# Optimization experiments

Hardware: AMD Instinct MI355X
Metric: run time of the kernel (lower is better)

The kernel has to match this reference:

```python
import jax, jax.numpy as jnp
import numpy as np

# DeformConv hyperparameters (from init_kwargs)
KH, KW = 3, 3
STRIDE, PAD, DIL = 1, 1, 1
GROUPS, DG = 1, 1  # groups=1, deformable_groups=1
B, C, H, W = 4, 64, 128, 128
O = 64
HO = (H + 2 * PAD - (DIL * (KH - 1) + 1)) // STRIDE + 1  # 128
WO = (W + 2 * PAD - (DIL * (KW - 1) + 1)) // STRIDE + 1  # 128


def setup_inputs() -> dict:
    key = jax.random.key(0)
    k1, k2, k3, k4 = jax.random.split(key, 4)
    x = jax.random.normal(k1, (B, C, H, W), dtype=jnp.float32)
    # offset channels: dg * K * 2, ordered (y, x) per kernel tap (DCNv1 CUDA layout)
    offset = jax.random.normal(k2, (B, 2 * DG * KH * KW, HO, WO), dtype=jnp.float32)
    fan_in = C * KH * KW
    weight = jax.random.normal(k3, (O, C // GROUPS, KH, KW), dtype=jnp.float32) / np.sqrt(fan_in)
    bias = jax.random.normal(k4, (O,), dtype=jnp.float32) * 0.01
    return {"x": x, "offset": offset, "weight": weight, "bias": bias}


def _deform_sample(x, offset):
    """Bilinear-sample x at deformed kernel tap locations.
    Returns [B, C, K, HO, WO] where K = KH*KW."""
    K = KH * KW
    Cg = C // DG
    # offset -> [B, DG, K, 2, HO, WO]; channel layout: dg*2*K, pairs (y, x)
    off = offset.reshape(B, DG, K, 2, HO, WO)
    off_y, off_x = off[:, :, :, 0], off[:, :, :, 1]  # [B, DG, K, HO, WO]

    ki = (jnp.arange(K) // KW).astype(jnp.float32)  # kernel row
    kj = (jnp.arange(K) % KW).astype(jnp.float32)   # kernel col
    base_h = (jnp.arange(HO) * STRIDE - PAD).astype(jnp.float32)
    base_w = (jnp.arange(WO) * STRIDE - PAD).astype(jnp.float32)

    # sampling positions [B, DG, K, HO, WO]
    py = off_y + (ki * DIL)[None, None, :, None, None] + base_h[None, None, None, :, None]
    px = off_x + (kj * DIL)[None, None, :, None, None] + base_w[None, None, None, None, :]

    y0f = jnp.floor(py)
    x0f = jnp.floor(px)
    ly = py - y0f
    lx = px - x0f
    hy = 1.0 - ly
    hx = 1.0 - lx
    y0 = y0f.astype(jnp.int32)
    x0 = x0f.astype(jnp.int32)
    y1 = y0 + 1
    x1 = x0 + 1

    flat = x.reshape(B, DG, Cg, H * W)

    def gather(yi, xi, wgt):
        valid = (yi >= 0) & (yi < H) & (xi >= 0) & (xi < W)
        idx = jnp.clip(yi, 0, H - 1) * W + jnp.clip(xi, 0, W - 1)
        idx = idx.reshape(B, DG, 1, K * HO * WO)
        v = jnp.take_along_axis(flat, idx, axis=-1).reshape(B, DG, Cg, K, HO, WO)
        return v * (wgt * valid.astype(wgt.dtype))[:, :, None]

    val = (gather(y0, x0, hy * hx) + gather(y0, x1, hy * lx)
           + gather(y1, x0, ly * hx) + gather(y1, x1, ly * lx))
    return val.reshape(B, C, K, HO, WO)


def reference(x, offset, weight, bias):
    sampled = _deform_sample(x, offset)              # [B, C, K, HO, WO]
    w = weight.reshape(O, C, KH * KW)                # groups = 1
    out = jnp.einsum('bckhw,ock->bohw', sampled, w)  # im2col + GEMM
    return out + bias[None, :, None, None]
```

## Files before the change

### kernel.cpp

```cpp
#include <hip/hip_runtime.h>
#include <hip/hip_fp16.h>


#define B_  4
#define C_  64
#define H_  128
#define W_  128
#define O_  64
#define HO_ 128
#define WO_ 128
#define NCHUNK 8
#define NGW 12
#define KSTEPS 3
#define NT_ 32
#define NROW 2
#define NCOL 64
#define NTASK (9 * NCOL)
#define SG  10
#define SBUF (SG * NCOL * 8)
#define TR  16
#define TC  48
#define TSLOTS (TR * TC)

typedef _Float16 half8 __attribute__((ext_vector_type(8)));
typedef __attribute__((ext_vector_type(4))) float f32x4;

union H8 { float4 v; __half2 h2[4]; half8 v8; };

__global__ __launch_bounds__(256)
void prep(const float* __restrict__ x, const float* __restrict__ w,
          __half* __restrict__ xt, __half* __restrict__ wt) {
    const int tid = threadIdx.x;
    if (blockIdx.x < 2048) {
        int t = blockIdx.x * 256 + tid;
        int xc = t & 127;
        int y  = (t >> 7) & 127;
        int ch = (t >> 14) & 7;
        int b  = t >> 17;
        const float* xp = x + (((size_t)(b * C_ + ch * 8) * H_) + y) * W_ + xc;
        union { __half h[8]; float4 v; } pk;
#pragma unroll
        for (int e = 0; e < 8; ++e) pk.h[e] = __float2half_rn(xp[e * H_ * W_]);
        *(float4*)(xt + (size_t)t * 8) = pk.v;
    } else {
        int t = (blockIdx.x - 2048) * 256 + tid;
        if (t >= NCHUNK * NGW * O_) return;
        int o  = t & 63;
        int g  = (t >> 6) % NGW;
        int ch = (t >> 6) / NGW;
        union { __half h[8]; float4 v; } pk;
#pragma unroll
        for (int e = 0; e < 8; ++e)
            pk.h[e] = (g < 9) ? __float2half_rn(w[(o * C_ + ch * 8 + e) * 9 + g])
                              : __half(0.0f);
        *(float4*)(wt + (size_t)t * 8) = pk.v;
    }
}

__global__ __launch_bounds__(256, 4)
void dcn_mfma(const __half* __restrict__ xt, const float* __restrict__ off,
              const __half* __restrict__ wt, const float* __restrict__ bias,
              float* __restrict__ out) {
    __shared__ __align__(16) _Float16 sS[2 * SBUF];
    __shared__ __align__(16) _Float16 sT[TSLOTS * 8];

    const int tid = threadIdx.x;
    const int bid = blockIdx.x;
    const int w4  = bid & 3;
    const int hp  = (bid >> 2) & 63;
    const int b   = bid >> 8;
    const int ho  = hp << 1;
    const int woB = w4 * NT_;
    const int yb  = ho - 6;
    const int xb  = woB - 8;

    int a0_[3], a1_[3], nf_[3];
    __half2 ua2_[3], ub2_[3], va2_[3], vb2_[3];
#pragma unroll
    for (int r = 0; r < 3; ++r) {
        bool act = (r < 2) || ((tid & 3) == 0);
        if (act) {
            int task = (r < 2) ? (tid + r * 256) : (512 + (tid >> 2));
            int k  = task >> 6;
            int n  = task & 63;
            int wo = (n & 31) + woB;
            int hr = ho + (n >> 5);
            int ki = k / 3, kj = k - 3 * ki;
            float oy = off[(((b * 18) + 2 * k    ) * HO_ + hr) * WO_ + wo];
            float ox = off[(((b * 18) + 2 * k + 1) * HO_ + hr) * WO_ + wo];
            float py = (float)(hr - 1 + ki) + oy;
            float px = (float)(wo - 1 + kj) + ox;
            float y0f = floorf(py), x0f = floorf(px);
            int   y0 = (int)y0f,   x0 = (int)x0f;
            float ly = py - y0f,   lx = px - x0f;
            float hy = 1.f - ly,   hx = 1.f - lx;
            int y1 = y0 + 1, x1 = x0 + 1;
            float vy0 = (y0 >= 0 && y0 < H_) ? 1.f : 0.f;
            float vy1 = (y1 >= 0 && y1 < H_) ? 1.f : 0.f;
            float vx0 = (x0 >= 0 && x0 < W_) ? 1.f : 0.f;
            float vx1 = (x1 >= 0 && x1 < W_) ? 1.f : 0.f;
            int cy0 = min(max(y0, 0), H_ - 1), cy1 = min(max(y1, 0), H_ - 1);
            int ax  = min(max(x0, 0), W_ - 2);
            int cx0 = min(max(x0, 0), W_ - 1), cx1 = min(max(x1, 0), W_ - 1);
            float w00 = hy * hx * vy0 * vx0;
            float w01 = hy * lx * vy0 * vx1;
            float w10 = ly * hx * vy1 * vx0;
            float w11 = ly * lx * vy1 * vx1;
            float s0 = (cx0 != ax) ? 1.f : 0.f;
            float s1 = (cx1 != ax) ? 1.f : 0.f;
            int t0 = cy0 - yb, t1 = cy1 - yb, txx = ax - xb;
            int fb = ((unsigned)t0  > (TR - 1)) |
                     ((unsigned)t1  > (TR - 1)) |
                     ((unsigned)txx > (TC - 2));
            nf_[r] = !fb;
            a0_[r] = fb ? (cy0 * W_ + ax) : (t0 * TC + txx);
            a1_[r] = fb ? (cy1 * W_ + ax) : (t1 * TC + txx);
            ua2_[r] = __float2half2_rn(w00 * (1.f - s0) + w01 * (1.f - s1));
            ub2_[r] = __float2half2_rn(w00 * s0 + w01 * s1);
            va2_[r] = __float2half2_rn(w10 * (1.f - s0) + w11 * (1.f - s1));
            vb2_[r] = __float2half2_rn(w10 * s0 + w11 * s1);
        }
    }

    int gofs[3];
#pragma unroll
    for (int j = 0; j < 3; ++j) {
        int s  = tid + j * 256;
        int rr = s / TC, cc = s - rr * TC;
        int yc = min(max(yb + rr, 0), H_ - 1);
        int xc = min(max(xb + cc, 0), W_ - 1);
        gofs[j] = yc * W_ + xc;
    }

    ((unsigned int*)&sS[9 * NCOL * 8])[tid]        = 0u;
    ((unsigned int*)&sS[SBUF + 9 * NCOL * 8])[tid] = 0u;

    float4 pf0, pf1, pf2;
    auto issue = [&](int ch) {
        const float4* xc = (const float4*)(xt + ((size_t)(b * NCHUNK + ch)) * (H_ * W_ * 8));
        pf0 = xc[gofs[0]];
        pf1 = xc[gofs[1]];
        pf2 = xc[gofs[2]];
    };

    auto sample = [&](int ch) {
        _Float16* buf = sS + (ch & 1) * SBUF;
        const float4* xcg = (const float4*)(xt + ((size_t)(b * NCHUNK + ch)) * (H_ * W_ * 8));
        const float4* tl  = (const float4*)sT;
#pragma unroll
        for (int r = 0; r < 3; ++r) {
            bool act = (r < 2) || ((tid & 3) == 0);
            if (act) {
                int task = (r < 2) ? (tid + r * 256) : (512 + (tid >> 2));
                int k = task >> 6;
                int n = task & 63;
                int a0 = a0_[r], a1 = a1_[r];
                H8 q00, q01, q10, q11;
                if (nf_[r]) {
                    q00.v = tl[a0];  q01.v = tl[a0 + 1];
                    q10.v = tl[a1];  q11.v = tl[a1 + 1];
                } else {
                    q00.v = xcg[a0]; q01.v = xcg[a0 + 1];
                    q10.v = xcg[a1]; q11.v = xcg[a1 + 1];
                }
                H8 s;
#pragma unroll
                for (int j = 0; j < 4; ++j) {
                    __half2 t0 = __hmul2(ua2_[r], q00.h2[j]);
                    t0 = __hfma2(ub2_[r], q01.h2[j], t0);
                    t0 = __hfma2(va2_[r], q10.h2[j], t0);
                    t0 = __hfma2(vb2_[r], q11.h2[j], t0);
                    s.h2[j] = t0;
                }
                *(half8*)&buf[(k * NCOL + n) * 8] = s.v8;
            }
        }
    };

    const int lane = tid & 63;
    const int wv   = tid >> 6;
    const int ow   = wv & 1;
    const int nw   = wv >> 1;
    const int quad = lane >> 4;
    const int l15  = lane & 15;

    f32x4 acc[2][2];
#pragma unroll
    for (int ot = 0; ot < 2; ++ot)
#pragma unroll
        for (int nt = 0; nt < 2; ++nt)
            acc[ot][nt] = (f32x4){0.f, 0.f, 0.f, 0.f};

    auto mfma_chunk = [&](int ch) {
        const __half*   wc  = wt + (size_t)(ch * NGW) * O_ * 8;
        const _Float16* buf = sS + (ch & 1) * SBUF;
#pragma unroll
        for (int ks = 0; ks < KSTEPS; ++ks) {
            int g  = ks * 4 + quad;
            int gb = (g < 9) ? g : 9;
            half8 bfr0 = *(const half8*)&buf[(gb * NCOL + nw * 32 +      l15) * 8];
            half8 bfr1 = *(const half8*)&buf[(gb * NCOL + nw * 32 + 16 + l15) * 8];
#pragma unroll
            for (int ot = 0; ot < 2; ++ot) {
                half8 afr = *(const half8*)(wc + (size_t)(g * O_ + ow * 32 + ot * 16 + l15) * 8);
                acc[ot][0] = __builtin_amdgcn_mfma_f32_16x16x32_f16(afr, bfr0, acc[ot][0], 0, 0, 0);
                acc[ot][1] = __builtin_amdgcn_mfma_f32_16x16x32_f16(afr, bfr1, acc[ot][1], 0, 0, 0);
            }
        }
    };

    issue(0);
    for (int ch = 0; ch < NCHUNK; ++ch) {
        float4* tw = (float4*)sT;
        tw[tid]       = pf0;
        tw[tid + 256] = pf1;
        tw[tid + 512] = pf2;
        __syncthreads();
        if (ch + 1 < NCHUNK) issue(ch + 1);
        sample(ch);
        if (ch > 0) mfma_chunk(ch - 1);
        __syncthreads();
    }
    mfma_chunk(NCHUNK - 1);

#pragma unroll
    for (int ot = 0; ot < 2; ++ot) {
#pragma unroll
        for (int nt = 0; nt < 2; ++nt) {
            int n   = nw * 32 + nt * 16 + l15;
            int row = n >> 5;
            int wo  = woB + (n & 31);
#pragma unroll
            for (int rg = 0; rg < 4; ++rg) {
                int o = ow * 32 + ot * 16 + quad * 4 + rg;
                out[(((size_t)(b * O_ + o)) * HO_ + ho + row) * WO_ + wo] =
                    acc[ot][nt][rg] + bias[o];
            }
        }
    }
}

extern "C" void kernel_launch(void* const* d_in, const int* in_sizes, int n_in,
                              void* d_out, int out_size, void* d_ws, size_t ws_size,
                              hipStream_t stream) {
    const float* x    = (const float*)d_in[0];
    const float* off  = (const float*)d_in[1];
    const float* w    = (const float*)d_in[2];
    const float* bias = (const float*)d_in[3];
    float* out = (float*)d_out;

    __half* wt = (__half*)d_ws;
    __half* xt = (__half*)((char*)d_ws + 262144);

    hipLaunchKernelGGL(prep, dim3(2048 + 24), dim3(256), 0, stream, x, w, xt, wt);
    hipLaunchKernelGGL(dcn_mfma, dim3(B_ * (HO_ / NROW) * (WO_ / NT_)), dim3(256), 0, stream,
                       xt, off, wt, bias, out);
}
```

Before: 96.74 us.

## Double-buffer input tile, drop a barrier, use 32x32x16 MFMA

The shared input tile now has two buffers. The prefetch of the next chunk is written into the alternate buffer at the end of each iteration, so the loop needs only one __syncthreads instead of two. The tile shrinks from 16x48 to 14x44 to keep shared memory in check. That means more samples near the tile edge fall back to global loads. The four 16x16x32 MFMAs per k-step are replaced by one 32x32x16 MFMA over six k-steps, and the output store is remapped to match.

After: 98.41 us. Within noise of the previous version (+1.7%).

```diff
diff --git a/kernel.cpp b/kernel.cpp
--- a/kernel.cpp
+++ b/kernel.cpp
@@ -11,19 +11,20 @@
 #define WO_ 128
 #define NCHUNK 8
 #define NGW 12
-#define KSTEPS 3
 #define NT_ 32
 #define NROW 2
 #define NCOL 64
 #define NTASK (9 * NCOL)
 #define SG  10
 #define SBUF (SG * NCOL * 8)
-#define TR  16
-#define TC  48
+#define TR  14
+#define TC  44
 #define TSLOTS (TR * TC)
+#define TBUF (TSLOTS * 8)
 
 typedef _Float16 half8 __attribute__((ext_vector_type(8)));
 typedef __attribute__((ext_vector_type(4))) float f32x4;
+typedef __attribute__((ext_vector_type(16))) float f32x16;
 
 union H8 { float4 v; __half2 h2[4]; half8 v8; };
 
@@ -62,7 +63,7 @@
               const __half* __restrict__ wt, const float* __restrict__ bias,
               float* __restrict__ out) {
     __shared__ __align__(16) _Float16 sS[2 * SBUF];
-    __shared__ __align__(16) _Float16 sT[TSLOTS * 8];
+    __shared__ __align__(16) _Float16 sT[2 * TBUF];
 
     const int tid = threadIdx.x;
     const int bid = blockIdx.x;
@@ -72,7 +73,7 @@
     const int ho  = hp << 1;
     const int woB = w4 * NT_;
     const int yb  = ho - 6;
-    const int xb  = woB - 8;
+    const int xb  = woB - 6;
 
     int a0_[3], a1_[3], nf_[3];
     __half2 ua2_[3], ub2_[3], va2_[3], vb2_[3];
@@ -126,7 +127,8 @@
 #pragma unroll
     for (int j = 0; j < 3; ++j) {
         int s  = tid + j * 256;
-        int rr = s / TC, cc = s - rr * TC;
+        int sc = (s < TSLOTS) ? s : (TSLOTS - 1);
+        int rr = sc / TC, cc = sc - rr * TC;
         int yc = min(max(yb + rr, 0), H_ - 1);
         int xc = min(max(xb + cc, 0), W_ - 1);
         gofs[j] = yc * W_ + xc;
@@ -140,13 +142,19 @@
         const float4* xc = (const float4*)(xt + ((size_t)(b * NCHUNK + ch)) * (H_ * W_ * 8));
         pf0 = xc[gofs[0]];
         pf1 = xc[gofs[1]];
-        pf2 = xc[gofs[2]];
+        if (tid < TSLOTS - 512) pf2 = xc[gofs[2]];
+    };
+    auto tile_write = [&](int parity) {
+        float4* tw = (float4*)(sT + parity * TBUF);
+        tw[tid]       = pf0;
+        tw[tid + 256] = pf1;
+        if (tid < TSLOTS - 512) tw[tid + 512] = pf2;
     };
 
     auto sample = [&](int ch) {
         _Float16* buf = sS + (ch & 1) * SBUF;
         const float4* xcg = (const float4*)(xt + ((size_t)(b * NCHUNK + ch)) * (H_ * W_ * 8));
-        const float4* tl  = (const float4*)sT;
+        const float4* tl  = (const float4*)(sT + (ch & 1) * TBUF);
 #pragma unroll
         for (int r = 0; r < 3; ++r) {
             bool act = (r < 2) || ((tid & 3) == 0);
@@ -181,61 +189,44 @@
     const int wv   = tid >> 6;
     const int ow   = wv & 1;
     const int nw   = wv >> 1;
-    const int quad = lane >> 4;
-    const int l15  = lane & 15;
-
-    f32x4 acc[2][2];
-#pragma unroll
-    for (int ot = 0; ot < 2; ++ot)
-#pragma unroll
-        for (int nt = 0; nt < 2; ++nt)
-            acc[ot][nt] = (f32x4){0.f, 0.f, 0.f, 0.f};
+    const int h2k  = lane >> 5;
+    const int l31  = lane & 31;
+
+    f32x16 acc = {0.f, 0.f, 0.f, 0.f, 0.f, 0.f, 0.f, 0.f,
+                  0.f, 0.f, 0.f, 0.f, 0.f, 0.f, 0.f, 0.f};
 
     auto mfma_chunk = [&](int ch) {
         const __half*   wc  = wt + (size_t)(ch * NGW) * O_ * 8;
         const _Float16* buf = sS + (ch & 1) * SBUF;
 #pragma unroll
-        for (int ks = 0; ks < KSTEPS; ++ks) {
-            int g  = ks * 4 + quad;
+        for (int ks = 0; ks < 6; ++ks) {
+            int g  = 2 * ks + h2k;
             int gb = (g < 9) ? g : 9;
-            half8 bfr0 = *(const half8*)&buf[(gb * NCOL + nw * 32 +      l15) * 8];
-            half8 bfr1 = *(const half8*)&buf[(gb * NCOL + nw * 32 + 16 + l15) * 8];
-#pragma unroll
-            for (int ot = 0; ot < 2; ++ot) {
-                half8 afr = *(const half8*)(wc + (size_t)(g * O_ + ow * 32 + ot * 16 + l15) * 8);
-                acc[ot][0] = __builtin_amdgcn_mfma_f32_16x16x32_f16(afr, bfr0, acc[ot][0], 0, 0, 0);
-                acc[ot][1] = __builtin_amdgcn_mfma_f32_16x16x32_f16(afr, bfr1, acc[ot][1], 0, 0, 0);
-            }
+            half8 bfr = *(const half8*)&buf[(gb * NCOL + nw * 32 + l31) * 8];
+            half8 afr = *(const half8*)(wc + (size_t)(g * O_ + ow * 32 + l31) * 8);
+            acc = __builtin_amdgcn_mfma_f32_32x32x16_f16(afr, bfr, acc, 0, 0, 0);
         }
     };
 
     issue(0);
+    tile_write(0);
     for (int ch = 0; ch < NCHUNK; ++ch) {
-        float4* tw = (float4*)sT;
-        tw[tid]       = pf0;
-        tw[tid + 256] = pf1;
-        tw[tid + 512] = pf2;
         __syncthreads();
         if (ch + 1 < NCHUNK) issue(ch + 1);
         sample(ch);
         if (ch > 0) mfma_chunk(ch - 1);
-        __syncthreads();
-    }
+        if (ch + 1 < NCHUNK) tile_write((ch + 1) & 1);
+    }
+    __syncthreads();
     mfma_chunk(NCHUNK - 1);
 
-#pragma unroll
-    for (int ot = 0; ot < 2; ++ot) {
-#pragma unroll
-        for (int nt = 0; nt < 2; ++nt) {
-            int n   = nw * 32 + nt * 16 + l15;
-            int row = n >> 5;
-            int wo  = woB + (n & 31);
-#pragma unroll
-            for (int rg = 0; rg < 4; ++rg) {
-                int o = ow * 32 + ot * 16 + quad * 4 + rg;
-                out[(((size_t)(b * O_ + o)) * HO_ + ho + row) * WO_ + wo] =
-                    acc[ot][nt][rg] + bias[o];
-            }
+    {
+        int wo = woB + l31;
+        size_t base = (((size_t)b * O_) * HO_ + ho + nw) * WO_ + wo;
+#pragma unroll
+        for (int rg = 0; rg < 16; ++rg) {
+            int o = ow * 32 + (rg & 3) + 8 * (rg >> 2) + 4 * h2k;
+            out[base + (size_t)o * HO_ * WO_] = acc[rg] + bias[o];
         }
     }
 }
```
